# Optimization experiments

Hardware: AMD Instinct MI355X
Metric: run time of the kernel (lower is better)

## Reference

```python
import jax, jax.numpy as jnp
import numpy as np

NUM_USERS = 200000
NUM_ITEMS = 100000
DIM = 64
NUM_LAYERS = 2
NUM_EDGES = 3200000
EPS = 1e-12  # F.normalize eps


def setup_inputs() -> dict:
    key = jax.random.key(0)
    ks = jax.random.split(key, 8)
    return {
        "user_emb": jax.random.normal(ks[0], (NUM_USERS, DIM), dtype=jnp.float32),
        "item_emb": jax.random.normal(ks[1], (NUM_ITEMS, DIM), dtype=jnp.float32),
        "Wu": jax.random.normal(ks[2], (NUM_LAYERS, DIM, 2 * DIM), dtype=jnp.float32) * 0.1,
        "Wi": jax.random.normal(ks[3], (NUM_LAYERS, DIM, 2 * DIM), dtype=jnp.float32) * 0.1,
        "u_idx": jax.random.randint(ks[4], (NUM_EDGES,), 0, NUM_USERS, dtype=jnp.int32),
        "i_idx": jax.random.randint(ks[5], (NUM_EDGES,), 0, NUM_ITEMS, dtype=jnp.int32),
        "w_u2i": jax.random.uniform(ks[6], (NUM_EDGES,), dtype=jnp.float32),
        "w_i2u": jax.random.uniform(ks[7], (NUM_EDGES,), dtype=jnp.float32),
    }


def _l2_normalize(x):
    # matches F.normalize(p=2, dim=1): x / max(||x||, eps)
    n = jnp.sqrt(jnp.sum(x * x, axis=1, keepdims=True))
    return x / jnp.maximum(n, EPS)


def _spmm(vals, rows, cols, h, num_rows):
    # (sparse [num_rows, num_cols]) @ h : gather rows of h at cols, scale, scatter-add
    msg = vals[:, None] * h[cols]  # [E, DIM]
    return jax.ops.segment_sum(msg, rows, num_segments=num_rows)


def reference(user_emb, item_emb, Wu, Wi, u_idx, i_idx, w_u2i, w_i2u):
    h_u, h_i = user_emb, item_emb
    for l in range(NUM_LAYERS):
        neigh_u = _spmm(w_u2i, u_idx, i_idx, h_i, NUM_USERS)   # adj_u2i @ h_i
        neigh_i = _spmm(w_i2u, i_idx, u_idx, h_u, NUM_ITEMS)   # adj_i2u @ h_u
        # Linear(2*dim -> dim, no bias): concat then x @ W.T
        h_u_new = jax.nn.relu(jnp.concatenate([h_u, neigh_u], axis=1) @ Wu[l].T)
        h_i_new = jax.nn.relu(jnp.concatenate([h_i, neigh_i], axis=1) @ Wi[l].T)
        h_u = _l2_normalize(h_u_new)
        h_i = _l2_normalize(h_i_new)
    return (h_u, h_i)
```

## Files before the change

### kernel.cpp

```cpp
#include <hip/hip_runtime.h>


#define N_USERS 200000
#define N_ITEMS 100000
#define N_EDGES 3200000
#define NB_U 782
#define NB_I 391

__global__ __launch_bounds__(256) void wprep_kernel(
    const float* __restrict__ Wu, const float* __restrict__ Wi,
    float* __restrict__ WuT, float* __restrict__ WiT)
{
    int idx = blockIdx.x * 256 + threadIdx.x;
    const float* src = Wu;
    float* dst = WuT;
    int i = idx;
    if (idx >= 16384) { src = Wi; dst = WiT; i = idx - 16384; }
    int l = i >> 13;
    int r = i & 8191;
    int j = r >> 7;
    int k = r & 127;
    dst[l * 8192 + k * 64 + j] = src[i];
}

__global__ __launch_bounds__(256) void hist_kernel(
    const int* __restrict__ u_idx, const int* __restrict__ i_idx,
    int* __restrict__ deg_u, int* __restrict__ deg_i,
    unsigned short* __restrict__ rank_u, unsigned short* __restrict__ rank_i)
{
    int t = blockIdx.x * 256 + threadIdx.x;
    if (t < N_EDGES) {
        rank_u[t] = (unsigned short)atomicAdd(&deg_u[u_idx[t]], 1);
    } else {
        int e = t - N_EDGES;
        rank_i[e] = (unsigned short)atomicAdd(&deg_i[i_idx[e]], 1);
    }
}

__global__ __launch_bounds__(256) void scanA_kernel(
    const int* __restrict__ deg_u, const int* __restrict__ deg_i,
    int* __restrict__ bsum_u, int* __restrict__ bsum_i)
{
    int b = blockIdx.x;
    const int* deg; int n; int* bs; int bb;
    if (b < NB_U) { deg = deg_u; n = N_USERS; bs = bsum_u; bb = b; }
    else          { deg = deg_i; n = N_ITEMS; bs = bsum_i; bb = b - NB_U; }
    int i = bb * 256 + threadIdx.x;
    int v = (i < n) ? deg[i] : 0;
    #pragma unroll
    for (int off = 1; off < 64; off <<= 1) v += __shfl_xor(v, off);
    __shared__ int ws4[4];
    int wv = threadIdx.x >> 6;
    if ((threadIdx.x & 63) == 0) ws4[wv] = v;
    __syncthreads();
    if (threadIdx.x == 0) bs[bb] = ws4[0] + ws4[1] + ws4[2] + ws4[3];
}

__global__ __launch_bounds__(1024) void scanB_kernel(
    const int* __restrict__ bsum_u, int* __restrict__ bpre_u,
    const int* __restrict__ bsum_i, int* __restrict__ bpre_i)
{
    __shared__ int s[1024];
    const int* src; int* dst; int n;
    if (blockIdx.x == 0) { src = bsum_u; dst = bpre_u; n = NB_U; }
    else                 { src = bsum_i; dst = bpre_i; n = NB_I; }
    int t = threadIdx.x;
    int v = (t < n) ? src[t] : 0;
    s[t] = v; __syncthreads();
    #pragma unroll
    for (int off = 1; off < 1024; off <<= 1) {
        int x = (t >= off) ? s[t - off] : 0;
        __syncthreads();
        s[t] += x;
        __syncthreads();
    }
    if (t < n) dst[t] = s[t] - v;
}

__global__ __launch_bounds__(256) void scanC_kernel(
    const int* __restrict__ deg_u, const int* __restrict__ deg_i,
    const int* __restrict__ bpre_u, const int* __restrict__ bpre_i,
    int* __restrict__ rowptr_u, int* __restrict__ rowptr_i)
{
    int b = blockIdx.x;
    const int* deg; int n; const int* bpre; int* rowptr; int bb;
    if (b < NB_U) { deg = deg_u; n = N_USERS; bpre = bpre_u; rowptr = rowptr_u; bb = b; }
    else          { deg = deg_i; n = N_ITEMS; bpre = bpre_i; rowptr = rowptr_i; bb = b - NB_U; }
    int t = threadIdx.x;
    int i = bb * 256 + t;
    int d = (i < n) ? deg[i] : 0;
    __shared__ int s[256];
    s[t] = d; __syncthreads();
    #pragma unroll
    for (int off = 1; off < 256; off <<= 1) {
        int x = (t >= off) ? s[t - off] : 0;
        __syncthreads();
        s[t] += x;
        __syncthreads();
    }
    int val = bpre[bb] + (s[t] - d);
    if (i < n) rowptr[i] = val;
    if (b == 0 && t == 0) { rowptr_u[N_USERS] = N_EDGES; rowptr_i[N_ITEMS] = N_EDGES; }
}

__global__ __launch_bounds__(256) void fill_kernel(
    const int* __restrict__ u_idx, const int* __restrict__ i_idx,
    const float* __restrict__ w_u2i, const float* __restrict__ w_i2u,
    const unsigned short* __restrict__ rank_u, const unsigned short* __restrict__ rank_i,
    const int* __restrict__ rowptr_u, const int* __restrict__ rowptr_i,
    uint2* __restrict__ edges_u, uint2* __restrict__ edges_i)
{
    const int part   = blockIdx.x & 7;
    const int slot   = blockIdx.x >> 3;
    const int nslots = gridDim.x >> 3;
    const int stride = nslots * 256;

    for (int e = slot * 256 + threadIdx.x; e < N_EDGES; e += stride) {
        int ru = u_idx[e];
        int ri = i_idx[e];
        if ((ru & 7) == part) {
            int p = rowptr_u[ru] + rank_u[e];
            edges_u[p] = make_uint2((unsigned)ri, __float_as_uint(w_u2i[e]));
        }
        if ((ri & 7) == part) {
            int p = rowptr_i[ri] + rank_i[e];
            edges_i[p] = make_uint2((unsigned)ru, __float_as_uint(w_i2u[e]));
        }
    }
}

__global__ __launch_bounds__(256, 4) void transform_fused_kernel(
    const float* __restrict__ hself_u, const float* __restrict__ hsrc_u,
    const int* __restrict__ rowptr_u, const uint2* __restrict__ edges_u,
    const float* __restrict__ WtU, float* __restrict__ out_u,
    const float* __restrict__ hself_i, const float* __restrict__ hsrc_i,
    const int* __restrict__ rowptr_i, const uint2* __restrict__ edges_i,
    const float* __restrict__ WtI, float* __restrict__ out_i,
    int nbu)
{
    __shared__ float Ws[64 * 64];
    __shared__ float Xs[64 * 68];
    __shared__ int   rp_s[65];

    const int tid = threadIdx.x;

    const float* hself; const float* hsrc; const int* rowptr;
    const uint2* edges; const float* Wt; float* out; int N; int bb;
    if ((int)blockIdx.x < nbu) {
        hself = hself_u; hsrc = hsrc_u; rowptr = rowptr_u; edges = edges_u;
        Wt = WtU; out = out_u; N = N_USERS; bb = blockIdx.x;
    } else {
        hself = hself_i; hsrc = hsrc_i; rowptr = rowptr_i; edges = edges_i;
        Wt = WtI; out = out_i; N = N_ITEMS; bb = blockIdx.x - nbu;
    }
    const int row0 = bb * 64;

    #pragma unroll
    for (int i = 0; i < 16; ++i) Ws[tid + i * 256] = Wt[tid + i * 256];
    #pragma unroll
    for (int i = 0; i < 16; ++i) {
        int idx = tid + i * 256;
        int rr = idx >> 6, cc = idx & 63;
        int gr = row0 + rr; if (gr > N - 1) gr = N - 1;
        Xs[rr * 68 + cc] = hself[gr * 64 + cc];
    }
    if (tid <= 64) rp_s[tid] = rowptr[min(row0 + tid, N)];
    __syncthreads();

    const int tr = tid >> 3;
    const int tc = tid & 7;
    const int r0 = 2 * tr;

    float acc[2][8];
    #pragma unroll
    for (int j = 0; j < 2; ++j)
        #pragma unroll
        for (int c = 0; c < 8; ++c) acc[j][c] = 0.f;

    #pragma unroll 8
    for (int k = 0; k < 64; ++k) {
        float a0 = Xs[r0 * 68 + k];
        float a1 = Xs[(r0 + 1) * 68 + k];
        float4 b0 = *(const float4*)&Ws[k * 64 + 8 * tc];
        float4 b1 = *(const float4*)&Ws[k * 64 + 8 * tc + 4];
        float b[8] = {b0.x, b0.y, b0.z, b0.w, b1.x, b1.y, b1.z, b1.w};
        #pragma unroll
        for (int c = 0; c < 8; ++c) {
            acc[0][c] = fmaf(a0, b[c], acc[0][c]);
            acc[1][c] = fmaf(a1, b[c], acc[1][c]);
        }
    }
    __syncthreads();

    {
        const float4* src = (const float4*)(Wt + 4096);
        float4* dst = (float4*)Ws;
        #pragma unroll
        for (int i = 0; i < 4; ++i) dst[tid + i * 256] = src[tid + i * 256];
        #pragma unroll
        for (int i = 0; i < 17; ++i) Xs[tid + i * 256] = 0.f;
    }
    __syncthreads();

    {
        const int wv = tid >> 6;
        const int ln = tid & 63;
        const int e0 = rp_s[0], e1 = rp_s[64];
        const int perw = (e1 - e0 + 3) >> 2;
        const int wsb  = e0 + wv * perw;
        const int web  = min(wsb + perw, e1);
        const int clen = (web - wsb + 7) >> 3;

        int   cs[8], ce[8], rr[8], nend[8];
        float gacc[8];
        uint2 ec[8];
        #pragma unroll
        for (int c = 0; c < 8; ++c) {
            cs[c] = wsb + c * clen;
            ce[c] = min(cs[c] + clen, web);
            gacc[c] = 0.f;
            int lo = 0, hi = 64;
            #pragma unroll
            for (int s = 0; s < 6; ++s) {
                int mid = (lo + hi) >> 1;
                bool go = rp_s[mid] <= cs[c];
                lo = go ? mid : lo;
                hi = go ? hi : mid;
            }
            rr[c] = lo; nend[c] = rp_s[lo + 1];
            ec[c] = edges[min(cs[c], N_EDGES - 1)];
        }

        #pragma unroll 1
        for (int it = 0; it < clen; ++it) {
            float hv[8], wg[8];
            #pragma unroll
            for (int c = 0; c < 8; ++c) {
                bool v = (cs[c] + it) < ce[c];
                wg[c] = v ? __uint_as_float(ec[c].y) : 0.f;
                hv[c] = hsrc[(int)ec[c].x * 64 + ln];
            }
            #pragma unroll
            for (int c = 0; c < 8; ++c)
                ec[c] = edges[min(cs[c] + it + 1, N_EDGES - 1)];
            #pragma unroll
            for (int c = 0; c < 8; ++c) {
                gacc[c] = fmaf(wg[c], hv[c], gacc[c]);
                int p   = cs[c] + it;
                int nxt = p + 1;
                if (p < ce[c] && (nxt == nend[c] || nxt == ce[c])) {
                    atomicAdd(&Xs[rr[c] * 68 + ln], gacc[c]);
                    gacc[c] = 0.f;
                    if (nxt == nend[c] && nxt < web) {
                        int r2 = rr[c];
                        while (r2 < 63 && rp_s[r2 + 1] <= nxt) ++r2;
                        rr[c] = r2; nend[c] = rp_s[r2 + 1];
                    }
                }
            }
        }
    }
    __syncthreads();

    #pragma unroll 8
    for (int k = 0; k < 64; ++k) {
        float a0 = Xs[r0 * 68 + k];
        float a1 = Xs[(r0 + 1) * 68 + k];
        float4 b0 = *(const float4*)&Ws[k * 64 + 8 * tc];
        float4 b1 = *(const float4*)&Ws[k * 64 + 8 * tc + 4];
        float b[8] = {b0.x, b0.y, b0.z, b0.w, b1.x, b1.y, b1.z, b1.w};
        #pragma unroll
        for (int c = 0; c < 8; ++c) {
            acc[0][c] = fmaf(a0, b[c], acc[0][c]);
            acc[1][c] = fmaf(a1, b[c], acc[1][c]);
        }
    }

    #pragma unroll
    for (int j = 0; j < 2; ++j) {
        float s = 0.f;
        #pragma unroll
        for (int c = 0; c < 8; ++c) {
            float v = fmaxf(acc[j][c], 0.f);
            acc[j][c] = v;
            s = fmaf(v, v, s);
        }
        s += __shfl_xor(s, 1);
        s += __shfl_xor(s, 2);
        s += __shfl_xor(s, 4);
        float nrm = sqrtf(s);
        float inv = 1.f / fmaxf(nrm, 1e-12f);
        int gr = row0 + r0 + j;
        if (gr < N) {
            float4 o0 = make_float4(acc[j][0]*inv, acc[j][1]*inv, acc[j][2]*inv, acc[j][3]*inv);
            float4 o1 = make_float4(acc[j][4]*inv, acc[j][5]*inv, acc[j][6]*inv, acc[j][7]*inv);
            float* p = out + gr * 64 + 8 * tc;
            *(float4*)p       = o0;
            *(float4*)(p + 4) = o1;
        }
    }
}

extern "C" void kernel_launch(void* const* d_in, const int* in_sizes, int n_in,
                              void* d_out, int out_size, void* d_ws, size_t ws_size,
                              hipStream_t stream)
{
    (void)in_sizes; (void)n_in; (void)out_size; (void)ws_size;

    const float* user_emb = (const float*)d_in[0];
    const float* item_emb = (const float*)d_in[1];
    const float* Wu       = (const float*)d_in[2];
    const float* Wi       = (const float*)d_in[3];
    const int*   u_idx    = (const int*)d_in[4];
    const int*   i_idx    = (const int*)d_in[5];
    const float* w_u2i    = (const float*)d_in[6];
    const float* w_i2u    = (const float*)d_in[7];
    float* out = (float*)d_out;

    float* ws      = (float*)d_ws;
    float* WuT     = ws;
    float* WiT     = WuT + 16384;
    float* hu1     = WiT + 16384;
    float* hi1     = hu1 + N_USERS * 64;
    uint2* edges_u = (uint2*)(hi1 + N_ITEMS * 64);
    uint2* edges_i = edges_u + N_EDGES;
    unsigned short* rank_u = (unsigned short*)(edges_i + N_EDGES);
    unsigned short* rank_i = rank_u + N_EDGES;
    int* rowptr_u = (int*)(rank_i + N_EDGES);
    int* rowptr_i = rowptr_u + (N_USERS + 1);
    int* deg_u    = rowptr_i + (N_ITEMS + 1);
    int* deg_i    = deg_u + N_USERS;
    int* bsum_u   = deg_i + N_ITEMS;
    int* bpre_u   = bsum_u + NB_U;
    int* bsum_i   = bpre_u + NB_U;
    int* bpre_i   = bsum_i + NB_I;

    const int tu_blocks = (N_USERS + 63) / 64;
    const int ti_blocks = (N_ITEMS + 63) / 64;
    const int e2_blocks = (2 * N_EDGES) / 256;

    wprep_kernel<<<128, 256, 0, stream>>>(Wu, Wi, WuT, WiT);
    hipMemsetAsync(deg_u, 0, (size_t)(N_USERS + N_ITEMS) * 4, stream);
    hist_kernel<<<e2_blocks, 256, 0, stream>>>(u_idx, i_idx, deg_u, deg_i, rank_u, rank_i);
    scanA_kernel<<<NB_U + NB_I, 256, 0, stream>>>(deg_u, deg_i, bsum_u, bsum_i);
    scanB_kernel<<<2, 1024, 0, stream>>>(bsum_u, bpre_u, bsum_i, bpre_i);
    scanC_kernel<<<NB_U + NB_I, 256, 0, stream>>>(deg_u, deg_i, bpre_u, bpre_i, rowptr_u, rowptr_i);
    fill_kernel<<<2048, 256, 0, stream>>>(u_idx, i_idx, w_u2i, w_i2u,
                                          rank_u, rank_i, rowptr_u, rowptr_i,
                                          edges_u, edges_i);

    transform_fused_kernel<<<tu_blocks + ti_blocks, 256, 0, stream>>>(
        user_emb, item_emb, rowptr_u, edges_u, WuT, hu1,
        item_emb, user_emb, rowptr_i, edges_i, WiT, hi1, tu_blocks);

    transform_fused_kernel<<<tu_blocks + ti_blocks, 256, 0, stream>>>(
        hu1, hi1, rowptr_u, edges_u, WuT + 8192, out,
        hi1, hu1, rowptr_i, edges_i, WiT + 8192, out + (size_t)N_USERS * 64, tu_blocks);
}
```

Measured before the change: 1.349 ms.

## Drop shared weight tile, read weights from cache, use packed FMA, interleave blocks

Removes the 16KB shared-memory weight buffer so the weights are read straight from global memory through cache, and raises the launch-bounds occupancy target from 4 to 7 blocks. The GEMM inner loops now use 2-wide float vectors, which allows packed FMA instructions. Blocks are remapped so user and item blocks alternate 2:1 across the grid, spreading the two workloads evenly over time. The trade-off is more global or L1 traffic for the weights and tighter register limits in exchange for higher occupancy.

```diff
diff --git a/kernel.cpp b/kernel.cpp
--- a/kernel.cpp
+++ b/kernel.cpp
@@ -6,6 +6,8 @@
 #define N_EDGES 3200000
 #define NB_U 782
 #define NB_I 391
+
+typedef float v2f __attribute__((ext_vector_type(2)));
 
 __global__ __launch_bounds__(256) void wprep_kernel(
     const float* __restrict__ Wu, const float* __restrict__ Wi,
@@ -129,7 +131,7 @@
     }
 }
 
-__global__ __launch_bounds__(256, 4) void transform_fused_kernel(
+__global__ __launch_bounds__(256, 7) void transform_fused_kernel(
     const float* __restrict__ hself_u, const float* __restrict__ hsrc_u,
     const int* __restrict__ rowptr_u, const uint2* __restrict__ edges_u,
     const float* __restrict__ WtU, float* __restrict__ out_u,
@@ -138,25 +140,37 @@
     const float* __restrict__ WtI, float* __restrict__ out_i,
     int nbu)
 {
-    __shared__ float Ws[64 * 64];
     __shared__ float Xs[64 * 68];
     __shared__ int   rp_s[65];
 
     const int tid = threadIdx.x;
 
+    const int nbt = (int)gridDim.x;
+    const int nbi = nbt - nbu;
+    int bid = (int)blockIdx.x;
+    int g = bid / 3, r = bid - 3 * g;
+    bool is_u; int bb;
+    if (r < 2) {
+        int cand = 2 * g + r;
+        if (cand < nbu) { is_u = true;  bb = cand; }
+        else            { is_u = false; bb = nbi - (nbt - bid); }
+    } else {
+        int cand = g;
+        if (cand < nbi) { is_u = false; bb = cand; }
+        else            { is_u = true;  bb = nbu - (nbt - bid); }
+    }
+
     const float* hself; const float* hsrc; const int* rowptr;
-    const uint2* edges; const float* Wt; float* out; int N; int bb;
-    if ((int)blockIdx.x < nbu) {
+    const uint2* edges; const float* Wt; float* out; int N;
+    if (is_u) {
         hself = hself_u; hsrc = hsrc_u; rowptr = rowptr_u; edges = edges_u;
-        Wt = WtU; out = out_u; N = N_USERS; bb = blockIdx.x;
+        Wt = WtU; out = out_u; N = N_USERS;
     } else {
         hself = hself_i; hsrc = hsrc_i; rowptr = rowptr_i; edges = edges_i;
-        Wt = WtI; out = out_i; N = N_ITEMS; bb = blockIdx.x - nbu;
+        Wt = WtI; out = out_i; N = N_ITEMS;
     }
     const int row0 = bb * 64;
 
-    #pragma unroll
-    for (int i = 0; i < 16; ++i) Ws[tid + i * 256] = Wt[tid + i * 256];
     #pragma unroll
     for (int i = 0; i < 16; ++i) {
         int idx = tid + i * 256;
@@ -171,35 +185,33 @@
     const int tc = tid & 7;
     const int r0 = 2 * tr;
 
-    float acc[2][8];
+    v2f acc2[2][4];
     #pragma unroll
     for (int j = 0; j < 2; ++j)
         #pragma unroll
-        for (int c = 0; c < 8; ++c) acc[j][c] = 0.f;
-
-    #pragma unroll 8
-    for (int k = 0; k < 64; ++k) {
-        float a0 = Xs[r0 * 68 + k];
-        float a1 = Xs[(r0 + 1) * 68 + k];
-        float4 b0 = *(const float4*)&Ws[k * 64 + 8 * tc];
-        float4 b1 = *(const float4*)&Ws[k * 64 + 8 * tc + 4];
-        float b[8] = {b0.x, b0.y, b0.z, b0.w, b1.x, b1.y, b1.z, b1.w};
-        #pragma unroll
-        for (int c = 0; c < 8; ++c) {
-            acc[0][c] = fmaf(a0, b[c], acc[0][c]);
-            acc[1][c] = fmaf(a1, b[c], acc[1][c]);
-        }
-    }
-    __syncthreads();
+        for (int c = 0; c < 4; ++c) acc2[j][c] = (v2f){0.f, 0.f};
 
     {
-        const float4* src = (const float4*)(Wt + 4096);
-        float4* dst = (float4*)Ws;
-        #pragma unroll
-        for (int i = 0; i < 4; ++i) dst[tid + i * 256] = src[tid + i * 256];
-        #pragma unroll
-        for (int i = 0; i < 17; ++i) Xs[tid + i * 256] = 0.f;
-    }
+        const float* Wg = Wt;
+        #pragma unroll 8
+        for (int k = 0; k < 64; ++k) {
+            float a0 = Xs[r0 * 68 + k];
+            float a1 = Xs[(r0 + 1) * 68 + k];
+            float4 b0 = *(const float4*)&Wg[k * 64 + 8 * tc];
+            float4 b1 = *(const float4*)&Wg[k * 64 + 8 * tc + 4];
+            v2f bv0 = {b0.x, b0.y}, bv1 = {b0.z, b0.w};
+            v2f bv2 = {b1.x, b1.y}, bv3 = {b1.z, b1.w};
+            v2f a0v = {a0, a0}, a1v = {a1, a1};
+            acc2[0][0] += a0v * bv0; acc2[0][1] += a0v * bv1;
+            acc2[0][2] += a0v * bv2; acc2[0][3] += a0v * bv3;
+            acc2[1][0] += a1v * bv0; acc2[1][1] += a1v * bv1;
+            acc2[1][2] += a1v * bv2; acc2[1][3] += a1v * bv3;
+        }
+    }
+    __syncthreads();
+
+    #pragma unroll
+    for (int i = 0; i < 17; ++i) Xs[tid + i * 256] = 0.f;
     __syncthreads();
 
     {
@@ -262,29 +274,34 @@
     }
     __syncthreads();
 
-    #pragma unroll 8
-    for (int k = 0; k < 64; ++k) {
-        float a0 = Xs[r0 * 68 + k];
-        float a1 = Xs[(r0 + 1) * 68 + k];
-        float4 b0 = *(const float4*)&Ws[k * 64 + 8 * tc];
-        float4 b1 = *(const float4*)&Ws[k * 64 + 8 * tc + 4];
-        float b[8] = {b0.x, b0.y, b0.z, b0.w, b1.x, b1.y, b1.z, b1.w};
-        #pragma unroll
-        for (int c = 0; c < 8; ++c) {
-            acc[0][c] = fmaf(a0, b[c], acc[0][c]);
-            acc[1][c] = fmaf(a1, b[c], acc[1][c]);
+    {
+        const float* Wg = Wt + 4096;
+        #pragma unroll 8
+        for (int k = 0; k < 64; ++k) {
+            float a0 = Xs[r0 * 68 + k];
+            float a1 = Xs[(r0 + 1) * 68 + k];
+            float4 b0 = *(const float4*)&Wg[k * 64 + 8 * tc];
+            float4 b1 = *(const float4*)&Wg[k * 64 + 8 * tc + 4];
+            v2f bv0 = {b0.x, b0.y}, bv1 = {b0.z, b0.w};
+            v2f bv2 = {b1.x, b1.y}, bv3 = {b1.z, b1.w};
+            v2f a0v = {a0, a0}, a1v = {a1, a1};
+            acc2[0][0] += a0v * bv0; acc2[0][1] += a0v * bv1;
+            acc2[0][2] += a0v * bv2; acc2[0][3] += a0v * bv3;
+            acc2[1][0] += a1v * bv0; acc2[1][1] += a1v * bv1;
+            acc2[1][2] += a1v * bv2; acc2[1][3] += a1v * bv3;
         }
     }
 
     #pragma unroll
     for (int j = 0; j < 2; ++j) {
+        float v[8];
+        v[0] = fmaxf(acc2[j][0].x, 0.f); v[1] = fmaxf(acc2[j][0].y, 0.f);
+        v[2] = fmaxf(acc2[j][1].x, 0.f); v[3] = fmaxf(acc2[j][1].y, 0.f);
+        v[4] = fmaxf(acc2[j][2].x, 0.f); v[5] = fmaxf(acc2[j][2].y, 0.f);
+        v[6] = fmaxf(acc2[j][3].x, 0.f); v[7] = fmaxf(acc2[j][3].y, 0.f);
         float s = 0.f;
         #pragma unroll
-        for (int c = 0; c < 8; ++c) {
-            float v = fmaxf(acc[j][c], 0.f);
-            acc[j][c] = v;
-            s = fmaf(v, v, s);
-        }
+        for (int c = 0; c < 8; ++c) s = fmaf(v[c], v[c], s);
         s += __shfl_xor(s, 1);
         s += __shfl_xor(s, 2);
         s += __shfl_xor(s, 4);
@@ -292,8 +309,8 @@
         float inv = 1.f / fmaxf(nrm, 1e-12f);
         int gr = row0 + r0 + j;
         if (gr < N) {
-            float4 o0 = make_float4(acc[j][0]*inv, acc[j][1]*inv, acc[j][2]*inv, acc[j][3]*inv);
-            float4 o1 = make_float4(acc[j][4]*inv, acc[j][5]*inv, acc[j][6]*inv, acc[j][7]*inv);
+            float4 o0 = make_float4(v[0]*inv, v[1]*inv, v[2]*inv, v[3]*inv);
+            float4 o1 = make_float4(v[4]*inv, v[5]*inv, v[6]*inv, v[7]*inv);
             float* p = out + gr * 64 + 8 * tc;
             *(float4*)p       = o0;
             *(float4*)(p + 4) = o1;
```

After: 5.160 ms. +282.6%, slower.
